# Kernel tuning notes

Hardware: AMD Instinct MI355X
Metric: run time of the kernel (lower is better)

The kernel has to match this reference:

```python
import jax, jax.numpy as jnp
import numpy as np

B, T, U = 4, 256, 100
H_ENC, H_DEC = 512, 512
INPUT_SIZE = H_ENC + H_DEC  # 1024, joint='concat'
INNER = 512
VOCAB = 1024


def setup_inputs() -> dict:
    key = jax.random.key(0)
    k1, k2, k3, k4, k5, k6 = jax.random.split(key, 6)
    s_in = 1.0 / np.sqrt(INPUT_SIZE)
    s_h = 1.0 / np.sqrt(INNER)
    return {
        "enc_state": jax.random.normal(k1, (B, T, H_ENC), dtype=jnp.float32),
        "dec_state": jax.random.normal(k2, (B, U, H_DEC), dtype=jnp.float32),
        # mlp[0]: Linear(input_size -> inner): W1 [inner, input_size], b1 [inner]
        "W1": jax.random.uniform(k3, (INNER, INPUT_SIZE), jnp.float32, -s_in, s_in),
        "b1": jax.random.uniform(k4, (INNER,), jnp.float32, -s_in, s_in),
        # mlp[2]: Linear(inner -> vocab): W2 [vocab, inner], b2 [vocab]
        "W2": jax.random.uniform(k5, (VOCAB, INNER), jnp.float32, -s_h, s_h),
        "b2": jax.random.uniform(k6, (VOCAB,), jnp.float32, -s_h, s_h),
    }


def reference(enc_state, dec_state, W1, b1, W2, b2):
    # joint='concat': concat([enc broadcast over U, dec broadcast over T], -1)
    # then Linear -> tanh -> Linear.
    # Mathematically identical fused form: split W1 into enc/dec column blocks,
    # project each at native size, broadcast-add.
    h_enc = H_ENC
    W1e = W1[:, :h_enc]   # [inner, H_enc]
    W1d = W1[:, h_enc:]   # [inner, H_dec]
    pe = jnp.einsum('bth,ih->bti', enc_state, W1e)  # [B,T,inner]
    pd = jnp.einsum('buh,ih->bui', dec_state, W1d)  # [B,U,inner]
    hidden = jnp.tanh(pe[:, :, None, :] + pd[:, None, :, :] + b1)  # [B,T,U,inner]
    joint = jnp.einsum('btui,vi->btuv', hidden, W2) + b2  # [B,T,U,vocab]
    return joint
```

## Files before the change

kernel.cpp:

```cpp
#include <hip/hip_runtime.h>
#include <hip/hip_bf16.h>

#define NB 4
#define NT 256
#define NU 100
#define NH 512
#define NI 512
#define NV 1024
#define MROWS (NB * NT * NU)

typedef __attribute__((ext_vector_type(4))) float f32x4;
typedef __attribute__((ext_vector_type(8))) __bf16 bf16x8;

static __device__ __forceinline__ unsigned int f2bf(float f) {
  unsigned int u = __float_as_uint(f);
  return (u + 0x7FFFu + ((u >> 16) & 1u)) >> 16;
}

static __device__ __forceinline__ float fast_tanh(float x) {
  float e = __expf(2.f * x);
  return 1.f - 2.f * __builtin_amdgcn_rcpf(1.f + e);
}

static __device__ __forceinline__ unsigned int cvt_pk_bf16(float lo, float hi) {
  unsigned int r;
  asm("v_cvt_pk_bf16_f32 %0, %1, %2" : "=v"(r) : "v"(lo), "v"(hi));
  return r;
}

static __device__ __forceinline__ void gload16(const void* g, void* l) {
  __builtin_amdgcn_global_load_lds(
      (const __attribute__((address_space(1))) unsigned int*)(g),
      (__attribute__((address_space(3))) unsigned int*)(l), 16, 0, 0);
}

__global__ __launch_bounds__(256) void proj_kernel(
    const float* __restrict__ enc, const float* __restrict__ dec,
    const float* __restrict__ W1, float* __restrict__ pe, float* __restrict__ pd) {
  __shared__ float As[64][17];
  __shared__ float Bs[64][17];
  const int bx = blockIdx.x;
  const float* A;
  float* P;
  int Mrows, colOff, row0;
  if (bx < 16) { A = enc; P = pe; Mrows = NB * NT; colOff = 0;  row0 = bx * 64; }
  else         { A = dec; P = pd; Mrows = NB * NU; colOff = NH; row0 = (bx - 16) * 64; }
  const int col0 = blockIdx.y * 64;
  const int tx = threadIdx.x;
  const int tr = tx >> 4, tc = tx & 15;
  const int lr = tx >> 2, lc = (tx & 3) * 4;
  float acc[4][4] = {};
  for (int k0 = 0; k0 < NH; k0 += 16) {
    float4 av = make_float4(0.f, 0.f, 0.f, 0.f);
    if (row0 + lr < Mrows)
      av = *(const float4*)(A + (size_t)(row0 + lr) * NH + k0 + lc);
    float4 bv = *(const float4*)(W1 + (size_t)(col0 + lr) * (NH + NH) + colOff + k0 + lc);
    As[lr][lc] = av.x; As[lr][lc + 1] = av.y; As[lr][lc + 2] = av.z; As[lr][lc + 3] = av.w;
    Bs[lr][lc] = bv.x; Bs[lr][lc + 1] = bv.y; Bs[lr][lc + 2] = bv.z; Bs[lr][lc + 3] = bv.w;
    __syncthreads();
#pragma unroll
    for (int kk = 0; kk < 16; ++kk) {
      float a4[4], b4[4];
#pragma unroll
      for (int i = 0; i < 4; ++i) { a4[i] = As[tr * 4 + i][kk]; b4[i] = Bs[tc * 4 + i][kk]; }
#pragma unroll
      for (int i = 0; i < 4; ++i)
#pragma unroll
        for (int j = 0; j < 4; ++j) acc[i][j] = fmaf(a4[i], b4[j], acc[i][j]);
    }
    __syncthreads();
  }
#pragma unroll
  for (int i = 0; i < 4; ++i) {
    int r = row0 + tr * 4 + i;
    if (r < Mrows) {
#pragma unroll
      for (int j = 0; j < 4; ++j)
        P[(size_t)r * NI + col0 + tc * 4 + j] = acc[i][j];
    }
  }
}

__global__ __launch_bounds__(256) void cvt_w2_frag_kernel(
    const float* __restrict__ W2, unsigned short* __restrict__ w2f) {
  int g = blockIdx.x * 256 + threadIdx.x;
  int lr = g & 15, lq = (g >> 4) & 3;
  int cb = (g >> 6) & 15, kt = (g >> 10) & 15, nt = (g >> 14) & 3;
  int v = nt * 256 + cb * 16 + lr;
  int k = kt * 32 + lq * 8;
  const float* src = W2 + (size_t)v * NI + k;
  float4 a = *(const float4*)src;
  float4 b = *(const float4*)(src + 4);
  uint4 o;
  o.x = f2bf(a.x) | (f2bf(a.y) << 16);
  o.y = f2bf(a.z) | (f2bf(a.w) << 16);
  o.z = f2bf(b.x) | (f2bf(b.y) << 16);
  o.w = f2bf(b.z) | (f2bf(b.w) << 16);
  *(uint4*)(w2f + (size_t)g * 8) = o;
}

__global__ __launch_bounds__(512, 4) void fused_joint_kernel(
    const float* __restrict__ pe, const float* __restrict__ pd,
    const float* __restrict__ b1, const unsigned short* __restrict__ w2f,
    const float* __restrict__ b2, float* __restrict__ out) {
  __shared__ unsigned char lds[49152];
  const int tx = threadIdx.x;
  const int nt = blockIdx.x & 3, mt = blockIdx.x >> 2;
  const int R0 = mt * 128, C0 = nt * 256;
  const int lane = tx & 63, wid = tx >> 6;
  const int wr = wid >> 2, wc = wid & 3;
  const int lr = lane & 15, lq = lane >> 4;

  const int arow = tx >> 2;
  const int kc = ((tx & 3) ^ ((tx >> 3) & 3)) * 8;
  int peOff, pdOff;
  {
    int g = R0 + arow;
    int b = g / (NT * NU);
    int rem = g - b * (NT * NU);
    int t = rem / NU;
    int u = rem - t * NU;
    peOff = (b * NT + t) * NI;
    pdOff = (b * NU + u) * NI;
  }
  const int afSw = ((lq ^ ((lr >> 1) & 3)) << 4);

#define STAGE_B(KT, BUF) do {                                                 \
    unsigned char* dB_ = lds + (BUF) * 24576 + 8192;                          \
    const unsigned char* src_ =                                               \
        (const unsigned char*)w2f + (((size_t)nt * 16 + (KT)) << 14);         \
    gload16(src_ + tx * 16, dB_ + tx * 16);                                   \
    gload16(src_ + (512 + tx) * 16, dB_ + (512 + tx) * 16);                   \
  } while (0)

  f32x4 acc[4][4];
#pragma unroll
  for (int mf = 0; mf < 4; ++mf)
#pragma unroll
    for (int nf = 0; nf < 4; ++nf)
#pragma unroll
      for (int z = 0; z < 4; ++z) acc[mf][nf][z] = 0.f;

  STAGE_B(0, 0);
  {
    const int k_ = kc;
    float4 p0 = *(const float4*)(pe + peOff + k_);
    float4 p1 = *(const float4*)(pe + peOff + k_ + 4);
    float4 q0 = *(const float4*)(pd + pdOff + k_);
    float4 q1 = *(const float4*)(pd + pdOff + k_ + 4);
    float4 c0 = *(const float4*)(b1 + k_);
    float4 c1 = *(const float4*)(b1 + k_ + 4);
    uint4 pk;
    pk.x = cvt_pk_bf16(fast_tanh(p0.x + q0.x + c0.x), fast_tanh(p0.y + q0.y + c0.y));
    pk.y = cvt_pk_bf16(fast_tanh(p0.z + q0.z + c0.z), fast_tanh(p0.w + q0.w + c0.w));
    pk.z = cvt_pk_bf16(fast_tanh(p1.x + q1.x + c1.x), fast_tanh(p1.y + q1.y + c1.y));
    pk.w = cvt_pk_bf16(fast_tanh(p1.z + q1.z + c1.z), fast_tanh(p1.w + q1.w + c1.w));
    *(uint4*)(lds + tx * 16) = pk;
  }
  __syncthreads();

  for (int kt = 0; kt < 16; ++kt) {
    const int cur = kt & 1;
    unsigned char* nbuf = lds + (cur ^ 1) * 24576;
    const unsigned char* Ab = lds + cur * 24576;
    const unsigned char* Bb = Ab + 8192;

    if (kt < 15) STAGE_B(kt + 1, cur ^ 1);

    float4 p0, p1, q0, q1, c0, c1;
    if (kt < 15) {
      const int k_ = (kt + 1) * 32 + kc;
      p0 = *(const float4*)(pe + peOff + k_);
      p1 = *(const float4*)(pe + peOff + k_ + 4);
      q0 = *(const float4*)(pd + pdOff + k_);
      q1 = *(const float4*)(pd + pdOff + k_ + 4);
      c0 = *(const float4*)(b1 + k_);
      c1 = *(const float4*)(b1 + k_ + 4);
    }

    bf16x8 af4[4];
#pragma unroll
    for (int mf = 0; mf < 4; ++mf)
      af4[mf] = *(const bf16x8*)(Ab + (wr * 64 + mf * 16 + lr) * 64 + afSw);

    __builtin_amdgcn_s_setprio(1);
#pragma unroll
    for (int nf = 0; nf < 4; ++nf) {
      bf16x8 bfv = *(const bf16x8*)(Bb + ((wc * 4 + nf) * 64 + lq * 16 + lr) * 16);
#pragma unroll
      for (int mf = 0; mf < 4; ++mf)
        acc[mf][nf] = __builtin_amdgcn_mfma_f32_16x16x32_bf16(
            af4[mf], bfv, acc[mf][nf], 0, 0, 0);
    }
    __builtin_amdgcn_s_setprio(0);

    if (kt < 15) {
      uint4 pk;
      pk.x = cvt_pk_bf16(fast_tanh(p0.x + q0.x + c0.x), fast_tanh(p0.y + q0.y + c0.y));
      pk.y = cvt_pk_bf16(fast_tanh(p0.z + q0.z + c0.z), fast_tanh(p0.w + q0.w + c0.w));
      pk.z = cvt_pk_bf16(fast_tanh(p1.x + q1.x + c1.x), fast_tanh(p1.y + q1.y + c1.y));
      pk.w = cvt_pk_bf16(fast_tanh(p1.z + q1.z + c1.z), fast_tanh(p1.w + q1.w + c1.w));
      *(uint4*)(nbuf + tx * 16) = pk;
      __syncthreads();
    }
  }
#undef STAGE_B

#pragma unroll
  for (int nf = 0; nf < 4; ++nf) {
    int col = C0 + wc * 64 + nf * 16 + lr;
    float bb = b2[col];
#pragma unroll
    for (int mf = 0; mf < 4; ++mf) {
#pragma unroll
      for (int j = 0; j < 4; ++j) {
        int grow = R0 + wr * 64 + mf * 16 + lq * 4 + j;
        out[(size_t)grow * NV + col] = acc[mf][nf][j] + bb;
      }
    }
  }
}

extern "C" void kernel_launch(void* const* d_in, const int* in_sizes, int n_in,
                              void* d_out, int out_size, void* d_ws, size_t ws_size,
                              hipStream_t stream) {
  const float* enc = (const float*)d_in[0];
  const float* dec = (const float*)d_in[1];
  const float* W1  = (const float*)d_in[2];
  const float* b1  = (const float*)d_in[3];
  const float* W2  = (const float*)d_in[4];
  const float* b2  = (const float*)d_in[5];
  float* out = (float*)d_out;
  char* ws = (char*)d_ws;

  float* pe = (float*)ws;
  float* pd = (float*)(ws + (2u << 20));
  unsigned short* w2f = (unsigned short*)(ws + (3u << 20));

  proj_kernel<<<dim3(23, 8), 256, 0, stream>>>(enc, dec, W1, pe, pd);
  cvt_w2_frag_kernel<<<256, 256, 0, stream>>>(W2, w2f);
  fused_joint_kernel<<<(MROWS / 128) * (NV / 256), 512, 0, stream>>>(
      pe, pd, b1, w2f, b2, out);
}
```

Baseline: 236.6 us.

## Compute hidden tile once per row block and stream W2 from registers

Each block now computes its full 128x512 bf16 hidden tile into LDS once and iterates over all vocab tiles, instead of recomputing tanh per column tile. W2 fragments are loaded directly from global into double-buffered registers rather than staged through LDS, which removes the per-k-step barriers. This trades away occupancy (128KB LDS per block, fewer blocks) and relies on L2 for W2 reuse.

```diff
diff --git a/kernel.cpp b/kernel.cpp
--- a/kernel.cpp
+++ b/kernel.cpp
@@ -26,12 +26,6 @@
   unsigned int r;
   asm("v_cvt_pk_bf16_f32 %0, %1, %2" : "=v"(r) : "v"(lo), "v"(hi));
   return r;
-}
-
-static __device__ __forceinline__ void gload16(const void* g, void* l) {
-  __builtin_amdgcn_global_load_lds(
-      (const __attribute__((address_space(1))) unsigned int*)(g),
-      (__attribute__((address_space(3))) unsigned int*)(l), 16, 0, 0);
 }
 
 __global__ __launch_bounds__(256) void proj_kernel(
@@ -99,126 +93,107 @@
   *(uint4*)(w2f + (size_t)g * 8) = o;
 }
 
-__global__ __launch_bounds__(512, 4) void fused_joint_kernel(
+__global__ __launch_bounds__(512, 2) void fused_joint_kernel(
     const float* __restrict__ pe, const float* __restrict__ pd,
     const float* __restrict__ b1, const unsigned short* __restrict__ w2f,
     const float* __restrict__ b2, float* __restrict__ out) {
-  __shared__ unsigned char lds[49152];
+  __shared__ unsigned char ldsA[131072];
   const int tx = threadIdx.x;
-  const int nt = blockIdx.x & 3, mt = blockIdx.x >> 2;
-  const int R0 = mt * 128, C0 = nt * 256;
+  const int R0 = blockIdx.x * 128;
   const int lane = tx & 63, wid = tx >> 6;
   const int wr = wid >> 2, wc = wid & 3;
   const int lr = lane & 15, lq = lane >> 4;
 
-  const int arow = tx >> 2;
-  const int kc = ((tx & 3) ^ ((tx >> 3) & 3)) * 8;
-  int peOff, pdOff;
-  {
-    int g = R0 + arow;
-    int b = g / (NT * NU);
-    int rem = g - b * (NT * NU);
+  const unsigned short* w2base = w2f + ((size_t)(wc * 4) * 64 + lq * 16 + lr) * 8;
+#define LOADB(DST, G) do {                                                    \
+    const unsigned short* s_ = w2base + ((size_t)(G) << 13);                  \
+    DST##0 = *(const bf16x8*)(s_);                                            \
+    DST##1 = *(const bf16x8*)(s_ + 512);                                      \
+    DST##2 = *(const bf16x8*)(s_ + 1024);                                     \
+    DST##3 = *(const bf16x8*)(s_ + 1536);                                     \
+  } while (0)
+
+  bf16x8 bA0, bA1, bA2, bA3, bB0, bB1, bB2, bB3;
+  LOADB(bA, 0);
+
+#pragma unroll 2
+  for (int pass = 0; pass < 16; ++pass) {
+    int idx = pass * 512 + tx;
+    int row = idx >> 6;
+    int g8 = idx & 63;
+    int i0 = g8 * 8;
+    int grow = R0 + row;
+    int b = grow / (NT * NU);
+    int rem = grow - b * (NT * NU);
     int t = rem / NU;
     int u = rem - t * NU;
-    peOff = (b * NT + t) * NI;
-    pdOff = (b * NU + u) * NI;
-  }
-  const int afSw = ((lq ^ ((lr >> 1) & 3)) << 4);
-
-#define STAGE_B(KT, BUF) do {                                                 \
-    unsigned char* dB_ = lds + (BUF) * 24576 + 8192;                          \
-    const unsigned char* src_ =                                               \
-        (const unsigned char*)w2f + (((size_t)nt * 16 + (KT)) << 14);         \
-    gload16(src_ + tx * 16, dB_ + tx * 16);                                   \
-    gload16(src_ + (512 + tx) * 16, dB_ + (512 + tx) * 16);                   \
-  } while (0)
-
-  f32x4 acc[4][4];
-#pragma unroll
-  for (int mf = 0; mf < 4; ++mf)
-#pragma unroll
-    for (int nf = 0; nf < 4; ++nf)
-#pragma unroll
-      for (int z = 0; z < 4; ++z) acc[mf][nf][z] = 0.f;
-
-  STAGE_B(0, 0);
-  {
-    const int k_ = kc;
-    float4 p0 = *(const float4*)(pe + peOff + k_);
-    float4 p1 = *(const float4*)(pe + peOff + k_ + 4);
-    float4 q0 = *(const float4*)(pd + pdOff + k_);
-    float4 q1 = *(const float4*)(pd + pdOff + k_ + 4);
-    float4 c0 = *(const float4*)(b1 + k_);
-    float4 c1 = *(const float4*)(b1 + k_ + 4);
+    const float* peP = pe + (size_t)(b * NT + t) * NI + i0;
+    const float* pdP = pd + (size_t)(b * NU + u) * NI + i0;
+    float4 p0 = *(const float4*)peP, p1 = *(const float4*)(peP + 4);
+    float4 q0 = *(const float4*)pdP, q1 = *(const float4*)(pdP + 4);
+    float4 c0 = *(const float4*)(b1 + i0), c1 = *(const float4*)(b1 + i0 + 4);
     uint4 pk;
     pk.x = cvt_pk_bf16(fast_tanh(p0.x + q0.x + c0.x), fast_tanh(p0.y + q0.y + c0.y));
     pk.y = cvt_pk_bf16(fast_tanh(p0.z + q0.z + c0.z), fast_tanh(p0.w + q0.w + c0.w));
     pk.z = cvt_pk_bf16(fast_tanh(p1.x + q1.x + c1.x), fast_tanh(p1.y + q1.y + c1.y));
     pk.w = cvt_pk_bf16(fast_tanh(p1.z + q1.z + c1.z), fast_tanh(p1.w + q1.w + c1.w));
-    *(uint4*)(lds + tx * 16) = pk;
+    *(uint4*)(ldsA + row * 1024 + ((g8 ^ (row & 7)) << 4)) = pk;
   }
   __syncthreads();
 
-  for (int kt = 0; kt < 16; ++kt) {
-    const int cur = kt & 1;
-    unsigned char* nbuf = lds + (cur ^ 1) * 24576;
-    const unsigned char* Ab = lds + cur * 24576;
-    const unsigned char* Bb = Ab + 8192;
-
-    if (kt < 15) STAGE_B(kt + 1, cur ^ 1);
-
-    float4 p0, p1, q0, q1, c0, c1;
-    if (kt < 15) {
-      const int k_ = (kt + 1) * 32 + kc;
-      p0 = *(const float4*)(pe + peOff + k_);
-      p1 = *(const float4*)(pe + peOff + k_ + 4);
-      q0 = *(const float4*)(pd + pdOff + k_);
-      q1 = *(const float4*)(pd + pdOff + k_ + 4);
-      c0 = *(const float4*)(b1 + k_);
-      c1 = *(const float4*)(b1 + k_ + 4);
-    }
-
-    bf16x8 af4[4];
-#pragma unroll
-    for (int mf = 0; mf < 4; ++mf)
-      af4[mf] = *(const bf16x8*)(Ab + (wr * 64 + mf * 16 + lr) * 64 + afSw);
-
-    __builtin_amdgcn_s_setprio(1);
-#pragma unroll
-    for (int nf = 0; nf < 4; ++nf) {
-      bf16x8 bfv = *(const bf16x8*)(Bb + ((wc * 4 + nf) * 64 + lq * 16 + lr) * 16);
-#pragma unroll
-      for (int mf = 0; mf < 4; ++mf)
-        acc[mf][nf] = __builtin_amdgcn_mfma_f32_16x16x32_bf16(
-            af4[mf], bfv, acc[mf][nf], 0, 0, 0);
-    }
-    __builtin_amdgcn_s_setprio(0);
-
-    if (kt < 15) {
-      uint4 pk;
-      pk.x = cvt_pk_bf16(fast_tanh(p0.x + q0.x + c0.x), fast_tanh(p0.y + q0.y + c0.y));
-      pk.y = cvt_pk_bf16(fast_tanh(p0.z + q0.z + c0.z), fast_tanh(p0.w + q0.w + c0.w));
-      pk.z = cvt_pk_bf16(fast_tanh(p1.x + q1.x + c1.x), fast_tanh(p1.y + q1.y + c1.y));
-      pk.w = cvt_pk_bf16(fast_tanh(p1.z + q1.z + c1.z), fast_tanh(p1.w + q1.w + c1.w));
-      *(uint4*)(nbuf + tx * 16) = pk;
-      __syncthreads();
-    }
-  }
-#undef STAGE_B
-
-#pragma unroll
-  for (int nf = 0; nf < 4; ++nf) {
-    int col = C0 + wc * 64 + nf * 16 + lr;
-    float bb = b2[col];
-#pragma unroll
-    for (int mf = 0; mf < 4; ++mf) {
-#pragma unroll
-      for (int j = 0; j < 4; ++j) {
-        int grow = R0 + wr * 64 + mf * 16 + lq * 4 + j;
-        out[(size_t)grow * NV + col] = acc[mf][nf][j] + bb;
-      }
-    }
-  }
+  f32x4 acc[4][4];
+#pragma unroll
+  for (int mf = 0; mf < 4; ++mf)
+#pragma unroll
+    for (int nf = 0; nf < 4; ++nf)
+#pragma unroll
+      for (int z = 0; z < 4; ++z) acc[mf][nf][z] = 0.f;
+
+#define COMPUTE(BV, G) do {                                                   \
+    const int kt_ = (G) & 15;                                                 \
+    bf16x8 af_[4];                                                            \
+    _Pragma("unroll")                                                         \
+    for (int mf = 0; mf < 4; ++mf) {                                          \
+      int row_ = wr * 64 + mf * 16 + lr;                                      \
+      af_[mf] = *(const bf16x8*)(ldsA + row_ * 1024 +                         \
+                                 (((kt_ * 4 + lq) ^ (lr & 7)) << 4));         \
+    }                                                                         \
+    __builtin_amdgcn_s_setprio(1);                                            \
+    _Pragma("unroll")                                                         \
+    for (int mf = 0; mf < 4; ++mf) {                                          \
+      acc[mf][0] = __builtin_amdgcn_mfma_f32_16x16x32_bf16(af_[mf], BV##0, acc[mf][0], 0, 0, 0); \
+      acc[mf][1] = __builtin_amdgcn_mfma_f32_16x16x32_bf16(af_[mf], BV##1, acc[mf][1], 0, 0, 0); \
+      acc[mf][2] = __builtin_amdgcn_mfma_f32_16x16x32_bf16(af_[mf], BV##2, acc[mf][2], 0, 0, 0); \
+      acc[mf][3] = __builtin_amdgcn_mfma_f32_16x16x32_bf16(af_[mf], BV##3, acc[mf][3], 0, 0, 0); \
+    }                                                                         \
+    __builtin_amdgcn_s_setprio(0);                                            \
+    if (kt_ == 15) {                                                          \
+      const int np_ = (G) >> 4;                                               \
+      _Pragma("unroll")                                                       \
+      for (int nf = 0; nf < 4; ++nf) {                                        \
+        int col_ = np_ * 256 + wc * 64 + nf * 16 + lr;                        \
+        float bb_ = b2[col_];                                                 \
+        _Pragma("unroll")                                                     \
+        for (int mf = 0; mf < 4; ++mf) {                                      \
+          _Pragma("unroll")                                                   \
+          for (int j = 0; j < 4; ++j) {                                       \
+            int grow_ = R0 + wr * 64 + mf * 16 + lq * 4 + j;                  \
+            out[(size_t)grow_ * NV + col_] = acc[mf][nf][j] + bb_;            \
+            acc[mf][nf][j] = 0.f;                                             \
+          }                                                                   \
+        }                                                                     \
+      }                                                                       \
+    }                                                                         \
+  } while (0)
+
+  for (int g = 0; g < 64; g += 2) {
+    LOADB(bB, g + 1);
+    COMPUTE(bA, g);
+    if (g + 2 < 64) LOADB(bA, g + 2);
+    COMPUTE(bB, g + 1);
+  }
+#undef COMPUTE
+#undef LOADB
 }
 
 extern "C" void kernel_launch(void* const* d_in, const int* in_sizes, int n_in,
@@ -239,6 +214,5 @@
 
   proj_kernel<<<dim3(23, 8), 256, 0, stream>>>(enc, dec, W1, pe, pd);
   cvt_w2_frag_kernel<<<256, 256, 0, stream>>>(W2, w2f);
-  fused_joint_kernel<<<(MROWS / 128) * (NV / 256), 512, 0, stream>>>(
-      pe, pd, b1, w2f, b2, out);
-}
+  fused_joint_kernel<<<MROWS / 128, 512, 0, stream>>>(pe, pd, b1, w2f, b2, out);
+}
```

Result: faster. 228.6 us (-3.4%).
